# Kernel optimization log

Hardware: AMD Instinct MI355X
Metric: run time of the kernel (lower is better)

## Reference

```python
import jax, jax.numpy as jnp
import numpy as np

B, H, W, C = 4, 64, 64, 32
M1 = M2 = 16
N = H * W          # 4096 grid nodes per sample
E = 131072         # edges (avg degree 32)
EDIM = 6           # edge feature dim
KMID = 64          # kernel MLP hidden width
EPS = 1e-5         # InstanceNorm eps


def _gelu(x):
    return jax.nn.gelu(x, approximate=False)  # torch nn.GELU default is exact erf


def _mlp(x, w1, b1, w2, b2):
    return _gelu(x @ w1 + b1) @ w2 + b2


def _inorm(x):
    # torch InstanceNorm2d(affine=False) applied to [B,H,W,C]: normalizes over last two dims
    m = x.mean(axis=(2, 3), keepdims=True)
    v = x.var(axis=(2, 3), keepdims=True)
    return (x - m) * jax.lax.rsqrt(v + EPS)


def _lin_init(k, fin, fout):
    lim = 1.0 / np.sqrt(fin)
    kw, kb = jax.random.split(k)
    w = jax.random.uniform(kw, (fin, fout), jnp.float32, -lim, lim)
    b = jax.random.uniform(kb, (fout,), jnp.float32, -lim, lim)
    return w, b


def setup_inputs() -> dict:
    key = jax.random.key(0)
    ks = jax.random.split(key, 14)
    s = 1.0 / (C * C)
    inp = {}
    inp['nodes'] = jax.random.normal(ks[0], (B, H, W, C), jnp.float32)
    inp['edge_index'] = jax.random.randint(ks[1], (2, E), 0, N, dtype=jnp.int64)
    inp['edge_attr'] = jax.random.uniform(ks[2], (E, EDIM), jnp.float32)
    # spectral conv complex weights, stored as real/imag float32 pairs
    inp['w1_re'] = s * jax.random.uniform(ks[3], (C, C, M1, M2), jnp.float32)
    inp['w1_im'] = s * jax.random.uniform(ks[4], (C, C, M1, M2), jnp.float32)
    inp['w2_re'] = s * jax.random.uniform(ks[5], (C, C, M1, M2), jnp.float32)
    inp['w2_im'] = s * jax.random.uniform(ks[6], (C, C, M1, M2), jnp.float32)
    # self.mlp : MLP(C, C, 2C)
    inp['mlp_w1'], inp['mlp_b1'] = _lin_init(ks[7], C, 2 * C)
    inp['mlp_w2'], inp['mlp_b2'] = _lin_init(ks[8], 2 * C, C)
    # self.w : MLP(C, C, 2C)
    inp['wm_w1'], inp['wm_b1'] = _lin_init(ks[9], C, 2 * C)
    inp['wm_w2'], inp['wm_b2'] = _lin_init(ks[10], 2 * C, C)
    # GNO kernel MLP : EDIM -> KMID -> C*C
    inp['ker_w1'], inp['ker_b1'] = _lin_init(ks[11], EDIM, KMID)
    inp['ker_w2'], inp['ker_b2'] = _lin_init(ks[12], KMID, C * C)
    # NNConv root weight and bias (PyG uniform(size) init with size=in_channels)
    lim = 1.0 / np.sqrt(C)
    kr, kb = jax.random.split(ks[13])
    inp['root'] = jax.random.uniform(kr, (C, C), jnp.float32, -lim, lim)
    inp['gbias'] = jax.random.uniform(kb, (C,), jnp.float32, -lim, lim)
    return inp


def reference(nodes, edge_index, edge_attr, w1_re, w1_im, w2_re, w2_im,
              mlp_w1, mlp_b1, mlp_w2, mlp_b2, wm_w1, wm_b1, wm_w2, wm_b2,
              ker_w1, ker_b1, ker_w2, ker_b2, root, gbias):
    x = _inorm(nodes)                                             # [B,H,W,C]

    # --- spectral conv branch ---
    x_ft = jnp.fft.rfftn(x, axes=(1, 2), norm='ortho')            # [B,H,W//2+1,C]
    w1 = (w1_re + 1j * w1_im).astype(jnp.complex64)
    w2 = (w2_re + 1j * w2_im).astype(jnp.complex64)
    top = jnp.einsum('bxyi,ioxy->bxyo', x_ft[:, :M1, :M2, :], w1)
    bot = jnp.einsum('bxyi,ioxy->bxyo', x_ft[:, -M1:, :M2, :], w2)
    out_ft = jnp.zeros((B, H, W // 2 + 1, C), jnp.complex64)
    out_ft = out_ft.at[:, :M1, :M2, :].set(top).at[:, -M1:, :M2, :].set(bot)
    x1 = jnp.fft.irfftn(out_ft, axes=(1, 2), s=(H, W), norm='ortho')
    x1 = _mlp(_inorm(x1), mlp_w1, mlp_b1, mlp_w2, mlp_b2)         # [B,H,W,C]

    # --- pointwise MLP branch ---
    x2 = _inorm(_mlp(x, wm_w1, wm_b1, wm_w2, wm_b2))              # [B,H,W,C]

    # --- edge-conditioned GNO branch ---
    x3 = x.reshape(B, N, C)
    wmat = _mlp(edge_attr, ker_w1, ker_b1, ker_w2, ker_b2).reshape(E, C, C)
    src, dst = edge_index[0], edge_index[1]
    msg = jnp.einsum('bec,eco->beo', x3[:, src, :], wmat)         # [B,E,C]
    agg = jnp.zeros((B, N, C), jnp.float32).at[:, dst, :].add(msg)
    x3 = agg + x3 @ root + gbias                                  # [B,N,C]

    return _gelu(x1 + x2 + x3.reshape(B, H, W, C))
```

## Files before the change

kernel.cpp:

```cpp
#include <hip/hip_runtime.h>

#define E_ 131072

typedef _Float16 half8 __attribute__((ext_vector_type(8)));
typedef float f32x4 __attribute__((ext_vector_type(4)));

__device__ __forceinline__ float gelu_f(float x) {
    return 0.5f * x * (1.0f + erff(x * 0.70710678118654752f));
}

#define TWOPI_64 (6.2831853071795864769f / 64.0f)

__device__ __forceinline__ void block_reduce2(float& s, float& s2, float* red) {
    #pragma unroll
    for (int off = 32; off > 0; off >>= 1) {
        s  += __shfl_down(s, off, 64);
        s2 += __shfl_down(s2, off, 64);
    }
    int lane = threadIdx.x & 63, wv = threadIdx.x >> 6;
    __syncthreads();
    if (lane == 0) { red[wv] = s; red[wv + 4] = s2; }
    __syncthreads();
    s  = red[0] + red[1] + red[2] + red[3];
    s2 = red[4] + red[5] + red[6] + red[7];
}

__device__ __forceinline__ void gno_body(int e0, float* sbufF, float* sB2, int* ssrc, int* sdst,
                                         const float* __restrict__ ea,
                                         const float* __restrict__ kw1, const float* __restrict__ kb1,
                                         const float* __restrict__ kb2,
                                         const _Float16* __restrict__ whi, const _Float16* __restrict__ wlo,
                                         const float* __restrict__ xn, const int* __restrict__ ei,
                                         float* __restrict__ agg) {
    _Float16* sxTh = (_Float16*)sbufF;
    int t = threadIdx.x;
    int lane = t & 63, wv = t >> 6, quad = lane >> 4, l15 = lane & 15;
    int eg = wv >> 1, t2 = wv & 1;

    if (t < 64) ssrc[t] = ei[e0 + t];
    else if (t < 128) sdst[t - 64] = ei[E_ + e0 + t - 64];
    for (int f = t; f < 1024; f += 256) sB2[f] = kb2[f];
    {
        int r = t >> 2, k0 = (t & 3) * 16;
        const float* ep = ea + (e0 + r) * 6;
        float e6[6];
        #pragma unroll
        for (int d = 0; d < 6; ++d) e6[d] = ep[d];
        #pragma unroll
        for (int kk = 0; kk < 16; ++kk) {
            int k = k0 + kk;
            float acc = kb1[k];
            #pragma unroll
            for (int d = 0; d < 6; ++d) acc += e6[d] * kw1[d * 64 + k];
            sbufF[r * 68 + k] = gelu_f(acc);
        }
    }
    __syncthreads();
    half8 ahi[2][2], alo[2][2];
    #pragma unroll
    for (int et = 0; et < 2; ++et) {
        #pragma unroll
        for (int kh = 0; kh < 2; ++kh) {
            const float* hp = sbufF + (eg * 32 + et * 16 + l15) * 68 + kh * 32 + quad * 8;
            float4 h0 = *(const float4*)hp;
            float4 h1 = *(const float4*)(hp + 4);
            float hv[8] = {h0.x, h0.y, h0.z, h0.w, h1.x, h1.y, h1.z, h1.w};
            half8 hh, hl;
            #pragma unroll
            for (int j = 0; j < 8; ++j) {
                _Float16 hi = (_Float16)hv[j];
                hh[j] = hi;
                hl[j] = (_Float16)(hv[j] - (float)hi);
            }
            ahi[et][kh] = hh;
            alo[et][kh] = hl;
        }
    }
    __syncthreads();
    {
        int b = t & 3, r = t >> 2;
        int s = ssrc[r];
        int pe = (r >> 5) * 32 + ((r >> 2) & 3) * 8 + ((r >> 4) & 1) * 4 + (r & 3);
        const float4* xp = (const float4*)(xn + (b * 4096 + s) * 32);
        _Float16* dp = sxTh + b * 2312 + pe;
        #pragma unroll
        for (int q = 0; q < 8; ++q) {
            float4 v = xp[q];
            dp[(q * 4 + 0) * 72] = (_Float16)v.x;
            dp[(q * 4 + 1) * 72] = (_Float16)v.y;
            dp[(q * 4 + 2) * 72] = (_Float16)v.z;
            dp[(q * 4 + 3) * 72] = (_Float16)v.w;
        }
    }
    __syncthreads();
    float msg[4][2][4];
    #pragma unroll
    for (int b = 0; b < 4; ++b)
        #pragma unroll
        for (int et = 0; et < 2; ++et)
            #pragma unroll
            for (int r = 0; r < 4; ++r) msg[b][et][r] = 0.f;

    for (int i = 0; i < 32; ++i) {
        float b2v = sB2[i * 32 + t2 * 16 + l15];
        int f0 = (i * 4 + t2 * 2) * 512 + lane * 8;
        half8 bhi0 = *(const half8*)(whi + f0);
        half8 bhi1 = *(const half8*)(whi + f0 + 512);
        half8 blo0 = *(const half8*)(wlo + f0);
        half8 blo1 = *(const half8*)(wlo + f0 + 512);
        f32x4 acc[2];
        #pragma unroll
        for (int et = 0; et < 2; ++et) {
            f32x4 ac = {b2v, b2v, b2v, b2v};
            ac = __builtin_amdgcn_mfma_f32_16x16x32_f16(ahi[et][0], bhi0, ac, 0, 0, 0);
            ac = __builtin_amdgcn_mfma_f32_16x16x32_f16(ahi[et][1], bhi1, ac, 0, 0, 0);
            ac = __builtin_amdgcn_mfma_f32_16x16x32_f16(ahi[et][0], blo0, ac, 0, 0, 0);
            ac = __builtin_amdgcn_mfma_f32_16x16x32_f16(ahi[et][1], blo1, ac, 0, 0, 0);
            ac = __builtin_amdgcn_mfma_f32_16x16x32_f16(alo[et][0], bhi0, ac, 0, 0, 0);
            ac = __builtin_amdgcn_mfma_f32_16x16x32_f16(alo[et][1], bhi1, ac, 0, 0, 0);
            acc[et] = ac;
        }
        #pragma unroll
        for (int b = 0; b < 4; ++b) {
            const half8 xv = *(const half8*)(sxTh + b * 2312 + i * 72 + eg * 32 + quad * 8);
            #pragma unroll
            for (int et = 0; et < 2; ++et) {
                msg[b][et][0] += (float)xv[et * 4 + 0] * acc[et][0];
                msg[b][et][1] += (float)xv[et * 4 + 1] * acc[et][1];
                msg[b][et][2] += (float)xv[et * 4 + 2] * acc[et][2];
                msg[b][et][3] += (float)xv[et * 4 + 3] * acc[et][3];
            }
        }
    }
    int o = t2 * 16 + l15;
    #pragma unroll
    for (int et = 0; et < 2; ++et) {
        #pragma unroll
        for (int r = 0; r < 4; ++r) {
            int row = eg * 32 + et * 16 + quad * 4 + r;
            int d = sdst[row];
            #pragma unroll
            for (int b = 0; b < 4; ++b) {
                atomicAdd(&agg[(b * 4096 + d) * 32 + o], msg[b][et][r]);
            }
        }
    }
}

__global__ __launch_bounds__(256, 4) void k_pre(const float* __restrict__ nodes,
                                                const float* __restrict__ w2,
                                                float* __restrict__ xn,
                                                float* __restrict__ agg,
                                                float* __restrict__ Gre, float* __restrict__ Gim,
                                                _Float16* __restrict__ whi, _Float16* __restrict__ wlo) {
    int t = threadIdx.x;
    if (blockIdx.x >= 256) {
        int g0 = (blockIdx.x - 256) * 512 + t;
        #pragma unroll 1
        for (int rep = 0; rep < 2; ++rep) {
            int g = g0 + rep * 256;
            int j = g & 7, l = (g >> 3) & 63, fid = g >> 9;
            int i = fid >> 2, t2 = (fid >> 1) & 1, kh = fid & 1;
            int quad = l >> 4, l15 = l & 15;
            int k = kh * 32 + quad * 8 + j;
            int n = i * 32 + t2 * 16 + l15;
            float v = w2[k * 1024 + n];
            _Float16 hi = (_Float16)v;
            whi[g] = hi;
            wlo[g] = (_Float16)(v - (float)hi);
        }
        return;
    }
    int bh = blockIdx.x;
    __shared__ float sx[2048];
    __shared__ float tc[64], ts[64];
    __shared__ float red[8];
    const float4* src = (const float4*)(nodes + bh * 2048);
    float4* dst = (float4*)(xn + bh * 2048);
    float4* az = (float4*)(agg + bh * 2048);
    if (t < 64) { float a = TWOPI_64 * t; tc[t] = cosf(a); ts[t] = sinf(a); }
    float4 v0 = src[t * 2], v1 = src[t * 2 + 1];
    float s  = v0.x + v0.y + v0.z + v0.w + v1.x + v1.y + v1.z + v1.w;
    float s2 = v0.x*v0.x + v0.y*v0.y + v0.z*v0.z + v0.w*v0.w
             + v1.x*v1.x + v1.y*v1.y + v1.z*v1.z + v1.w*v1.w;
    block_reduce2(s, s2, red);
    float mean = s * (1.0f / 2048.0f);
    float var  = s2 * (1.0f / 2048.0f) - mean * mean;
    float sc = rsqrtf(var + 1e-5f);
    v0.x = (v0.x - mean) * sc; v0.y = (v0.y - mean) * sc;
    v0.z = (v0.z - mean) * sc; v0.w = (v0.w - mean) * sc;
    v1.x = (v1.x - mean) * sc; v1.y = (v1.y - mean) * sc;
    v1.z = (v1.z - mean) * sc; v1.w = (v1.w - mean) * sc;
    dst[t * 2] = v0; dst[t * 2 + 1] = v1;
    float4 z = {0.f, 0.f, 0.f, 0.f};
    az[t * 2] = z; az[t * 2 + 1] = z;
    ((float4*)sx)[t * 2] = v0;
    ((float4*)sx)[t * 2 + 1] = v1;
    __syncthreads();
    #pragma unroll 1
    for (int rep = 0; rep < 2; ++rep) {
        int oi = rep * 256 + t;
        int ky = oi >> 5, i = oi & 31;
        float re = 0.f, im = 0.f;
        #pragma unroll 8
        for (int w = 0; w < 64; ++w) {
            float v = sx[w * 32 + i];
            int m = (ky * w) & 63;
            re += v * tc[m];
            im -= v * ts[m];
        }
        Gre[bh * 512 + oi] = re;
        Gim[bh * 512 + oi] = im;
    }
}

__global__ __launch_bounds__(256, 4) void k_g1(
        const float* __restrict__ Gre, const float* __restrict__ Gim,
        const float* __restrict__ w1re, const float* __restrict__ w1im,
        const float* __restrict__ w2re, const float* __restrict__ w2im,
        float* __restrict__ Yr, float* __restrict__ Yi,
        const float* __restrict__ ww1, const float* __restrict__ wb1,
        const float* __restrict__ ww2, const float* __restrict__ wb2,
        float* __restrict__ osum,
        const float* __restrict__ ea,
        const float* __restrict__ kw1, const float* __restrict__ kb1,
        const float* __restrict__ kb2,
        const _Float16* __restrict__ whi, const _Float16* __restrict__ wlo,
        const float* __restrict__ xn,
        const int* __restrict__ ei,
        float* __restrict__ agg) {
    __shared__ __align__(16) float U[5648];
    __shared__ int ssrc[64], sdst[64];
    int t = threadIdx.x;

    if (blockIdx.x < 128) {
        float* tc  = U;
        float* ts  = U + 64;
        float* sXr = U + 128;
        float* sXi = U + 656;
        int bid = blockIdx.x;
        int b = bid >> 5, kxi = bid & 31;
        int kx = kxi + (kxi < 16 ? 0 : 32);
        int x = kxi & 15;
        const float* wre = (kxi < 16) ? w1re : w2re;
        const float* wim = (kxi < 16) ? w1im : w2im;
        if (t < 64) { float a = TWOPI_64 * t; tc[t] = cosf(a); ts[t] = sinf(a); }
        __syncthreads();
        #pragma unroll 1
        for (int rep = 0; rep < 2; ++rep) {
            int oi = rep * 256 + t;
            int ky = oi >> 5, i = oi & 31;
            float re = 0.f, im = 0.f;
            #pragma unroll 8
            for (int h = 0; h < 64; ++h) {
                int gidx = (b * 64 + h) * 512 + ky * 32 + i;
                float gr = Gre[gidx], gi = Gim[gidx];
                int m = (kx * h) & 63;
                float c = tc[m], sv = ts[m];
                re += gr * c + gi * sv;
                im += gi * c - gr * sv;
            }
            sXr[ky * 33 + i] = re;
            sXi[ky * 33 + i] = im;
        }
        __syncthreads();
        #pragma unroll 1
        for (int rep = 0; rep < 2; ++rep) {
            int oi = rep * 256 + t;
            int ky = oi & 15, o = oi >> 4;
            float re = 0.f, im = 0.f;
            #pragma unroll 4
            for (int i = 0; i < 32; ++i) {
                float xr = sXr[ky * 33 + i], xi = sXi[ky * 33 + i];
                int widx = (i * 32 + o) * 256 + x * 16 + ky;
                float wr = wre[widx], wi = wim[widx];
                re += xr * wr - xi * wi;
                im += xr * wi + xi * wr;
            }
            Yr[bid * 512 + ky * 32 + o] = re;
            Yi[bid * 512 + ky * 32 + o] = im;
        }
        return;
    }
    if (blockIdx.x < 384) {
        int bh = blockIdx.x - 128;
        float* red = U;
        float* sX = U + 8;
        _Float16* sHh = (_Float16*)(U + 2120);
        for (int f = t; f < 2048; f += 256) sX[(f >> 5) * 33 + (f & 31)] = xn[bh * 2048 + f];
        __syncthreads();
        #pragma unroll 1
        for (int rep = 0; rep < 16; ++rep) {
            int idx = rep * 256 + t;
            int w = idx >> 6, k = idx & 63;
            float acc = wb1[k];
            #pragma unroll 4
            for (int c = 0; c < 32; ++c) acc += sX[w * 33 + c] * ww1[c * 64 + k];
            sHh[w * 72 + k] = (_Float16)gelu_f(acc);
        }
        __syncthreads();
        float s = 0.f, s2 = 0.f;
        #pragma unroll 1
        for (int rep = 0; rep < 8; ++rep) {
            int idx = rep * 256 + t;
            int w = idx >> 5, o = idx & 31;
            float acc = wb2[o];
            #pragma unroll 4
            for (int k = 0; k < 64; ++k) acc += (float)sHh[w * 72 + k] * ww2[k * 32 + o];
            sX[w * 33 + o] = acc;
            s += acc; s2 += acc * acc;
        }
        block_reduce2(s, s2, red);
        float mean = s * (1.0f / 2048.0f);
        float sc = rsqrtf(s2 * (1.0f / 2048.0f) - mean * mean + 1e-5f);
        #pragma unroll 1
        for (int rep = 0; rep < 8; ++rep) {
            int idx = rep * 256 + t;
            int w = idx >> 5, o = idx & 31;
            osum[bh * 2048 + idx] = (sX[w * 33 + o] - mean) * sc;
        }
        return;
    }
    gno_body((blockIdx.x - 384) * 64, U, U + 4624, ssrc, sdst,
             ea, kw1, kb1, kb2, whi, wlo, xn, ei, agg);
}

__global__ __launch_bounds__(256, 4) void k_g2(
        const float* __restrict__ Yr, const float* __restrict__ Yi,
        const float* __restrict__ mw1, const float* __restrict__ mb1,
        const float* __restrict__ mw2, const float* __restrict__ mb2,
        float* __restrict__ osum,
        const float* __restrict__ ea,
        const float* __restrict__ kw1, const float* __restrict__ kb1,
        const float* __restrict__ kb2,
        const _Float16* __restrict__ whi, const _Float16* __restrict__ wlo,
        const float* __restrict__ xn,
        const int* __restrict__ ei,
        float* __restrict__ agg) {
    __shared__ __align__(16) float U[5648];
    __shared__ int ssrc[64], sdst[64];
    int t = threadIdx.x;

    if (blockIdx.x < 256) {
        int bh = blockIdx.x;
        int b = bh >> 6, h = bh & 63;
        float* tc  = U;
        float* ts  = U + 64;
        float* red = U + 128;
        float* sZr = U + 136;
        float* sZi = U + 664;
        float* sP  = U + 1192;
        _Float16* sHh = (_Float16*)(U + 3304);
        if (t < 64) { float a = TWOPI_64 * t; tc[t] = cosf(a); ts[t] = sinf(a); }
        __syncthreads();
        #pragma unroll 1
        for (int rep = 0; rep < 2; ++rep) {
            int oi = rep * 256 + t;
            int ky = oi >> 5, o = oi & 31;
            float re = 0.f, im = 0.f;
            #pragma unroll 4
            for (int kxi = 0; kxi < 32; ++kxi) {
                int kx = kxi + (kxi < 16 ? 0 : 32);
                int m = (kx * h) & 63;
                float c = tc[m], sv = ts[m];
                int yidx = (b * 32 + kxi) * 512 + ky * 32 + o;
                float yr = Yr[yidx], yi = Yi[yidx];
                re += yr * c - yi * sv;
                im += yr * sv + yi * c;
            }
            sZr[ky * 33 + o] = re;
            sZi[ky * 33 + o] = im;
        }
        __syncthreads();
        float s = 0.f, s2 = 0.f;
        #pragma unroll 1
        for (int rep = 0; rep < 8; ++rep) {
            int idx = rep * 256 + t;
            int w = idx >> 5, o = idx & 31;
            float acc = sZr[o];
            #pragma unroll
            for (int ky = 1; ky < 16; ++ky) {
                int m = (ky * w) & 63;
                acc += 2.0f * (sZr[ky * 33 + o] * tc[m] - sZi[ky * 33 + o] * ts[m]);
            }
            acc *= (1.0f / 4096.0f);
            sP[w * 33 + o] = acc;
            s += acc; s2 += acc * acc;
        }
        block_reduce2(s, s2, red);
        float mean = s * (1.0f / 2048.0f);
        float sc = rsqrtf(s2 * (1.0f / 2048.0f) - mean * mean + 1e-5f);
        #pragma unroll 1
        for (int rep = 0; rep < 8; ++rep) {
            int idx = rep * 256 + t;
            int w = idx >> 5, o = idx & 31;
            sP[w * 33 + o] = (sP[w * 33 + o] - mean) * sc;
        }
        __syncthreads();
        #pragma unroll 1
        for (int rep = 0; rep < 16; ++rep) {
            int idx = rep * 256 + t;
            int w = idx >> 6, k = idx & 63;
            float acc = mb1[k];
            #pragma unroll 4
            for (int c = 0; c < 32; ++c) acc += sP[w * 33 + c] * mw1[c * 64 + k];
            sHh[w * 72 + k] = (_Float16)gelu_f(acc);
        }
        __syncthreads();
        #pragma unroll 1
        for (int rep = 0; rep < 8; ++rep) {
            int idx = rep * 256 + t;
            int w = idx >> 5, o = idx & 31;
            float acc = mb2[o];
            #pragma unroll 4
            for (int k = 0; k < 64; ++k) acc += (float)sHh[w * 72 + k] * mw2[k * 32 + o];
            osum[bh * 2048 + idx] += acc;
        }
        return;
    }
    gno_body((1024 + blockIdx.x - 256) * 64, U, U + 4624, ssrc, sdst,
             ea, kw1, kb1, kb2, whi, wlo, xn, ei, agg);
}

__global__ __launch_bounds__(256, 4) void k_final(const float* __restrict__ osum, const float* __restrict__ agg,
                                                  const float* __restrict__ xn, const float* __restrict__ root,
                                                  const float* __restrict__ gbias, float* __restrict__ out) {
    int bh = blockIdx.x >> 2, q = blockIdx.x & 3;
    int base = bh * 2048 + q * 512;
    int t = threadIdx.x;
    __shared__ float sX[16 * 33];
    __shared__ float sR[1024];
    for (int f = t; f < 512; f += 256) sX[(f >> 5) * 33 + (f & 31)] = xn[base + f];
    for (int f = t; f < 1024; f += 256) sR[f] = root[f];
    __syncthreads();
    #pragma unroll 1
    for (int rep = 0; rep < 2; ++rep) {
        int idx = rep * 256 + t;
        int w = idx >> 5, o = idx & 31;
        float acc = gbias[o] + osum[base + idx] + agg[base + idx];
        #pragma unroll 4
        for (int c = 0; c < 32; ++c) acc += sX[w * 33 + c] * sR[c * 32 + o];
        out[base + idx] = gelu_f(acc);
    }
}

extern "C" void kernel_launch(void* const* d_in, const int* in_sizes, int n_in,
                              void* d_out, int out_size, void* d_ws, size_t ws_size,
                              hipStream_t stream) {
    (void)in_sizes; (void)n_in; (void)out_size; (void)ws_size;
    const float* nodes  = (const float*)d_in[0];
    const int*   eidx   = (const int*)d_in[1];
    const float* eattr  = (const float*)d_in[2];
    const float* w1re   = (const float*)d_in[3];
    const float* w1im   = (const float*)d_in[4];
    const float* w2re   = (const float*)d_in[5];
    const float* w2im   = (const float*)d_in[6];
    const float* mlp_w1 = (const float*)d_in[7];
    const float* mlp_b1 = (const float*)d_in[8];
    const float* mlp_w2 = (const float*)d_in[9];
    const float* mlp_b2 = (const float*)d_in[10];
    const float* wm_w1  = (const float*)d_in[11];
    const float* wm_b1  = (const float*)d_in[12];
    const float* wm_w2  = (const float*)d_in[13];
    const float* wm_b2  = (const float*)d_in[14];
    const float* ker_w1 = (const float*)d_in[15];
    const float* ker_b1 = (const float*)d_in[16];
    const float* ker_w2 = (const float*)d_in[17];
    const float* ker_b2 = (const float*)d_in[18];
    const float* root   = (const float*)d_in[19];
    const float* gbias  = (const float*)d_in[20];
    float* out = (float*)d_out;

    char* ws = (char*)d_ws;
    size_t off = 0;
    auto alloc = [&](size_t bytes) {
        void* p = ws + off;
        off += (bytes + 255) & ~(size_t)255;
        return p;
    };
    float* xn   = (float*)alloc(524288 * 4);
    float* agg  = (float*)alloc(524288 * 4);
    float* osum = (float*)alloc(524288 * 4);
    float* Gre  = (float*)alloc(131072 * 4);
    float* Gim  = (float*)alloc(131072 * 4);
    float* Yr   = (float*)alloc(65536 * 4);
    float* Yi   = (float*)alloc(65536 * 4);
    _Float16* whi = (_Float16*)alloc(65536 * 2);
    _Float16* wlo = (_Float16*)alloc(65536 * 2);

    k_pre<<<384, 256, 0, stream>>>(nodes, ker_w2, xn, agg, Gre, Gim, whi, wlo);
    k_g1<<<1408, 256, 0, stream>>>(Gre, Gim, w1re, w1im, w2re, w2im, Yr, Yi,
                                   wm_w1, wm_b1, wm_w2, wm_b2, osum,
                                   eattr, ker_w1, ker_b1, ker_b2, whi, wlo, xn, eidx, agg);
    k_g2<<<1280, 256, 0, stream>>>(Yr, Yi, mlp_w1, mlp_b1, mlp_w2, mlp_b2, osum,
                                   eattr, ker_w1, ker_b1, ker_b2, whi, wlo, xn, eidx, agg);
    k_final<<<1024, 256, 0, stream>>>(osum, agg, xn, root, gbias, out);
}
```

Before: 248.1 us.

## Double-buffer GNO kernel weights in LDS via async global_load_lds

The GNO edge loop no longer reads the hi/lo fp16 kernel-MLP weight slices straight from global memory each iteration. It now streams them into a double-buffered LDS stage with global_load_lds, prefetching slice i+1 while slice i is consumed, and synchronises with waitcnt plus block barriers. It also raises MFMA priority with setprio and vectorises the message accumulation. This costs about 16 KB of extra LDS per block, which may lower occupancy, and adds two barriers per iteration.

Result: slower. 265.8 us (+7.1%).

```diff
diff --git a/kernel.cpp b/kernel.cpp
--- a/kernel.cpp
+++ b/kernel.cpp
@@ -3,6 +3,7 @@
 #define E_ 131072
 
 typedef _Float16 half8 __attribute__((ext_vector_type(8)));
+typedef _Float16 half4v __attribute__((ext_vector_type(4)));
 typedef float f32x4 __attribute__((ext_vector_type(4)));
 
 __device__ __forceinline__ float gelu_f(float x) {
@@ -10,6 +11,13 @@
 }
 
 #define TWOPI_64 (6.2831853071795864769f / 64.0f)
+
+__device__ __forceinline__ void gload_lds16(const void* g, void* l) {
+    __builtin_amdgcn_global_load_lds(
+        (__attribute__((address_space(1))) const void*)g,
+        (__attribute__((address_space(3))) void*)l,
+        16, 0, 0);
+}
 
 __device__ __forceinline__ void block_reduce2(float& s, float& s2, float* red) {
     #pragma unroll
@@ -25,7 +33,8 @@
     s2 = red[4] + red[5] + red[6] + red[7];
 }
 
-__device__ __forceinline__ void gno_body(int e0, float* sbufF, float* sB2, int* ssrc, int* sdst,
+__device__ __forceinline__ void gno_body(int e0, float* sbufF, float* sB2, float* sStage,
+                                         int* ssrc, int* sdst,
                                          const float* __restrict__ ea,
                                          const float* __restrict__ kw1, const float* __restrict__ kb1,
                                          const float* __restrict__ kb2,
@@ -33,9 +42,13 @@
                                          const float* __restrict__ xn, const int* __restrict__ ei,
                                          float* __restrict__ agg) {
     _Float16* sxTh = (_Float16*)sbufF;
+    _Float16* sBst = (_Float16*)sStage;
     int t = threadIdx.x;
     int lane = t & 63, wv = t >> 6, quad = lane >> 4, l15 = lane & 15;
     int eg = wv >> 1, t2 = wv & 1;
+
+    gload_lds16((const char*)whi + t * 16, (char*)sBst + t * 16);
+    gload_lds16((const char*)wlo + t * 16, (char*)sBst + 4096 + t * 16);
 
     if (t < 64) ssrc[t] = ei[e0 + t];
     else if (t < 128) sdst[t - 64] = ei[E_ + e0 + t - 64];
@@ -93,22 +106,35 @@
         }
     }
     __syncthreads();
-    float msg[4][2][4];
+
+    f32x4 msgv[4][2];
     #pragma unroll
     for (int b = 0; b < 4; ++b)
         #pragma unroll
-        for (int et = 0; et < 2; ++et)
-            #pragma unroll
-            for (int r = 0; r < 4; ++r) msg[b][et][r] = 0.f;
-
+        for (int et = 0; et < 2; ++et) msgv[b][et] = (f32x4){0.f, 0.f, 0.f, 0.f};
+
+    #pragma unroll 1
     for (int i = 0; i < 32; ++i) {
+        const _Float16* sb = sBst + (i & 1) * 4096;
+        if (i < 31) {
+            _Float16* nb = sBst + ((i + 1) & 1) * 4096;
+            gload_lds16((const char*)whi + (i + 1) * 4096 + t * 16, (char*)nb + t * 16);
+            gload_lds16((const char*)wlo + (i + 1) * 4096 + t * 16, (char*)nb + 4096 + t * 16);
+            asm volatile("s_waitcnt vmcnt(2)" ::: "memory");
+        } else {
+            asm volatile("s_waitcnt vmcnt(0)" ::: "memory");
+        }
+        __builtin_amdgcn_sched_barrier(0);
+        __builtin_amdgcn_s_barrier();
+        __builtin_amdgcn_sched_barrier(0);
+
         float b2v = sB2[i * 32 + t2 * 16 + l15];
-        int f0 = (i * 4 + t2 * 2) * 512 + lane * 8;
-        half8 bhi0 = *(const half8*)(whi + f0);
-        half8 bhi1 = *(const half8*)(whi + f0 + 512);
-        half8 blo0 = *(const half8*)(wlo + f0);
-        half8 blo1 = *(const half8*)(wlo + f0 + 512);
+        half8 bhi0 = *(const half8*)(sb + t2 * 1024 + lane * 8);
+        half8 bhi1 = *(const half8*)(sb + t2 * 1024 + 512 + lane * 8);
+        half8 blo0 = *(const half8*)(sb + 2048 + t2 * 1024 + lane * 8);
+        half8 blo1 = *(const half8*)(sb + 2048 + t2 * 1024 + 512 + lane * 8);
         f32x4 acc[2];
+        __builtin_amdgcn_s_setprio(1);
         #pragma unroll
         for (int et = 0; et < 2; ++et) {
             f32x4 ac = {b2v, b2v, b2v, b2v};
@@ -120,17 +146,18 @@
             ac = __builtin_amdgcn_mfma_f32_16x16x32_f16(alo[et][1], bhi1, ac, 0, 0, 0);
             acc[et] = ac;
         }
+        __builtin_amdgcn_s_setprio(0);
         #pragma unroll
         for (int b = 0; b < 4; ++b) {
             const half8 xv = *(const half8*)(sxTh + b * 2312 + i * 72 + eg * 32 + quad * 8);
-            #pragma unroll
-            for (int et = 0; et < 2; ++et) {
-                msg[b][et][0] += (float)xv[et * 4 + 0] * acc[et][0];
-                msg[b][et][1] += (float)xv[et * 4 + 1] * acc[et][1];
-                msg[b][et][2] += (float)xv[et * 4 + 2] * acc[et][2];
-                msg[b][et][3] += (float)xv[et * 4 + 3] * acc[et][3];
-            }
-        }
+            half4v h0 = {xv[0], xv[1], xv[2], xv[3]};
+            half4v h1 = {xv[4], xv[5], xv[6], xv[7]};
+            msgv[b][0] += __builtin_convertvector(h0, f32x4) * acc[0];
+            msgv[b][1] += __builtin_convertvector(h1, f32x4) * acc[1];
+        }
+        __builtin_amdgcn_sched_barrier(0);
+        __builtin_amdgcn_s_barrier();
+        __builtin_amdgcn_sched_barrier(0);
     }
     int o = t2 * 16 + l15;
     #pragma unroll
@@ -141,7 +168,7 @@
             int d = sdst[row];
             #pragma unroll
             for (int b = 0; b < 4; ++b) {
-                atomicAdd(&agg[(b * 4096 + d) * 32 + o], msg[b][et][r]);
+                atomicAdd(&agg[(b * 4096 + d) * 32 + o], msgv[b][et][r]);
             }
         }
     }
@@ -229,7 +256,7 @@
         const float* __restrict__ xn,
         const int* __restrict__ ei,
         float* __restrict__ agg) {
-    __shared__ __align__(16) float U[5648];
+    __shared__ __align__(16) float U[9744];
     __shared__ int ssrc[64], sdst[64];
     int t = threadIdx.x;
 
@@ -321,7 +348,7 @@
         }
         return;
     }
-    gno_body((blockIdx.x - 384) * 64, U, U + 4624, ssrc, sdst,
+    gno_body((blockIdx.x - 384) * 64, U, U + 4624, U + 5648, ssrc, sdst,
              ea, kw1, kb1, kb2, whi, wlo, xn, ei, agg);
 }
 
@@ -337,7 +364,7 @@
         const float* __restrict__ xn,
         const int* __restrict__ ei,
         float* __restrict__ agg) {
-    __shared__ __align__(16) float U[5648];
+    __shared__ __align__(16) float U[9744];
     __shared__ int ssrc[64], sdst[64];
     int t = threadIdx.x;
 
@@ -418,7 +445,7 @@
         }
         return;
     }
-    gno_body((1024 + blockIdx.x - 256) * 64, U, U + 4624, ssrc, sdst,
+    gno_body((1024 + blockIdx.x - 256) * 64, U, U + 4624, U + 5648, ssrc, sdst,
              ea, kw1, kb1, kb2, whi, wlo, xn, ei, agg);
 }
 
```
